# Kernel tuning notes

Hardware: AMD Instinct MI355X
Metric: run time of the kernel (lower is better)

Reference implementation:

```python
import jax, jax.numpy as jnp
import numpy as np

NS, NV, HE = 16, 8, 32          # scalar channels, vector (l=1) channels, edge hidden
D = NS + 3 * NV                  # flat irreps feature dim = 40
WN = NS*NS + NV*NS + NS*NV + NV*NV + NV*NV  # per-edge TP weight numel = 640
N_NODES, N_EDGES = 10000, 160000
C110 = 1.0 / np.sqrt(3.0)        # CG norm for 1o x 1o -> 0e (dot)
C111 = 1.0 / np.sqrt(2.0)        # CG norm for 1o x 1o -> 1o (cross)
EPS = 1e-5
_OFF = np.cumsum([0, NS*NS, NV*NS, NS*NV, NV*NV, NV*NV])


def _split(x):
    return x[:, :NS], x[:, NS:].reshape(x.shape[0], NV, 3)


def _flat(s, v):
    return jnp.concatenate([s, v.reshape(v.shape[0], -1)], axis=-1)


def _irreps_linear(x, Ws, Wv):
    s, v = _split(x)
    return s @ Ws, jnp.einsum('nid,io->nod', v, Wv)


def _mlp(x, w1, b1, w2, b2):
    return jax.nn.relu(x @ w1 + b1) @ w2 + b2


def _tp(x_s, x_v, sh, w):
    # equivariant tensor product (feat 16x0e+8x1o) x (sh 1x0e+1x1o) -> (16x0e+8x1o)
    E = x_s.shape[0]
    sh_s, sh_v = sh[:, 0], sh[:, 1:4]
    w1 = w[:, _OFF[0]:_OFF[1]].reshape(E, NS, NS)  # 0e x 0e -> 0e
    w2 = w[:, _OFF[1]:_OFF[2]].reshape(E, NV, NS)  # 1o x 1o -> 0e (dot)
    w3 = w[:, _OFF[2]:_OFF[3]].reshape(E, NS, NV)  # 0e x 1o -> 1o
    w4 = w[:, _OFF[3]:_OFF[4]].reshape(E, NV, NV)  # 1o x 0e -> 1o
    w5 = w[:, _OFF[4]:_OFF[5]].reshape(E, NV, NV)  # 1o x 1o -> 1o (cross)
    dot = jnp.einsum('eid,ed->ei', x_v, sh_v)
    cross = jnp.cross(x_v, sh_v[:, None, :])
    out_s = (jnp.einsum('eio,ei->eo', w1, x_s * sh_s[:, None])
             + C110 * jnp.einsum('eio,ei->eo', w2, dot))
    out_v = (jnp.einsum('eio,ei,ed->eod', w3, x_s, sh_v)
             + jnp.einsum('eio,eid->eod', w4, x_v * sh_s[:, None, None])
             + C111 * jnp.einsum('eio,eid->eod', w5, cross))
    return out_s, out_v


def _batchnorm(x, w_s, b_s, w_v):
    # e3nn-style BatchNorm: standard BN on scalars, norm-normalization on vectors
    s, v = _split(x)
    mu, var = s.mean(0), s.var(0)
    s = (s - mu) / jnp.sqrt(var + EPS) * w_s + b_s
    norm = (v * v).mean(-1).mean(0)  # [NV]
    v = v / jnp.sqrt(norm + EPS)[None, :, None] * w_v[None, :, None]
    return _flat(s, v)


def setup_inputs() -> dict:
    key = jax.random.key(0)
    ks = jax.random.split(key, 12)
    g = lambda i, shape, sc=1.0: jax.random.normal(ks[i], shape, jnp.float32) * sc
    return {
        'atom_features': g(0, (N_NODES, D)),
        'edge_features': g(1, (N_EDGES, HE)),
        'edge_sh': g(2, (N_EDGES, 4)),
        'Wq_s': g(3, (NS, NS), 1.0 / np.sqrt(NS)),
        'Wq_v': g(4, (NV, NV), 1.0 / np.sqrt(NV)),
        'k_w1': g(5, (HE, HE), 1.0 / np.sqrt(HE)), 'k_b1': jnp.zeros((HE,), jnp.float32),
        'k_w2': g(6, (HE, WN), 1.0 / np.sqrt(HE)), 'k_b2': jnp.zeros((WN,), jnp.float32),
        'v_w1': g(7, (HE, HE), 1.0 / np.sqrt(HE)), 'v_b1': jnp.zeros((HE,), jnp.float32),
        'v_w2': g(8, (HE, WN), 1.0 / np.sqrt(HE)), 'v_b2': jnp.zeros((WN,), jnp.float32),
        'bn_w_s': jnp.ones((NS,), jnp.float32), 'bn_b_s': jnp.zeros((NS,), jnp.float32),
        'bn_w_v': jnp.ones((NV,), jnp.float32),
        'edge_index': jax.random.randint(ks[9], (2, N_EDGES), 0, N_NODES),
    }


def reference(atom_features, edge_features, edge_sh, Wq_s, Wq_v,
              k_w1, k_b1, k_w2, k_b2, v_w1, v_b1, v_w2, v_b2,
              bn_w_s, bn_b_s, bn_w_v, edge_index):
    edge_dst, edge_src = edge_index[0], edge_index[1]
    q = _flat(*_irreps_linear(atom_features, Wq_s, Wq_v))[edge_src]     # [E, D]
    x_s, x_v = _split(atom_features[edge_dst])
    k = _flat(*_tp(x_s, x_v, edge_sh, _mlp(edge_features, k_w1, k_b1, k_w2, k_b2)))
    v = _flat(*_tp(x_s, x_v, edge_sh, _mlp(edge_features, v_w1, v_b1, v_w2, v_b2)))
    attn = jnp.sum(q * k, axis=-1)                                       # [E]
    m = jax.ops.segment_max(attn, edge_src, num_segments=N_NODES)
    m = jnp.where(jnp.isfinite(m), m, 0.0)
    e = jnp.exp(attn - m[edge_src])
    denom = jax.ops.segment_sum(e, edge_src, num_segments=N_NODES)
    a = e / denom[edge_src]
    upd = jax.ops.segment_sum(v * a[:, None], edge_src, num_segments=N_NODES)
    out = _batchnorm(atom_features + upd, bn_w_s, bn_b_s, bn_w_v)
    return out, edge_features
```

## Files before the change

### kernel.cpp

```cpp
#include <hip/hip_runtime.h>
#include <hip/hip_bf16.h>

typedef unsigned short u16;
typedef unsigned int u32;
typedef _Float16 h16;

#define NNODES 10000
#define NEDGES 160000

#define C110 0.57735026918962576f
#define C111 0.70710678118654752f

typedef __attribute__((ext_vector_type(8))) _Float16 half8;
typedef __attribute__((ext_vector_type(4))) float f32x4;

__device__ int   g_isf32;
__device__ float g_q[NNODES * 40];
__device__ float g_x[NNODES * 40];
__device__ float g_stats64[64][40];
__device__ u16   g_vb16[(size_t)NEDGES * 40];
__device__ u32   g_cnt8[8 * NNODES];
__device__ int2  g_bucket2[(size_t)NNODES * 128];
__device__ h16   g_w1hk[1024], g_w1lk[1024], g_w1hv[1024], g_w1lv[1024];
__device__ __align__(16) h16 g_w2k[640 * 32];
__device__ __align__(16) h16 g_w2v[640 * 32];
__device__ float g_b1k[32], g_b1v[32], g_b2k[640], g_b2v[640];

__device__ __forceinline__ float bf2f(u16 v) {
    return __uint_as_float(((u32)v) << 16);
}
__device__ __forceinline__ u32 f2bfbits(float f) {
    u32 u = __float_as_uint(f);
    u32 r = 0x7FFFu + ((u >> 16) & 1u);
    return (u + r) >> 16;
}
__device__ __forceinline__ u32 pack2(float a, float b) {
    return f2bfbits(a) | (f2bfbits(b) << 16);
}
__device__ __forceinline__ float ldx(const void* p, size_t i, int f32) {
    return f32 ? ((const float*)p)[i] : bf2f(((const u16*)p)[i]);
}
__device__ __forceinline__ void split2h(float v, h16& hi, h16& lo) {
    h16 h = (h16)v;
    hi = h;
    lo = (h16)(v - (float)h);
}
__device__ __forceinline__ void unp8(uint4 v, float* x) {
    x[0] = bf2f((u16)(v.x & 0xffffu)); x[1] = bf2f((u16)(v.x >> 16));
    x[2] = bf2f((u16)(v.y & 0xffffu)); x[3] = bf2f((u16)(v.y >> 16));
    x[4] = bf2f((u16)(v.z & 0xffffu)); x[5] = bf2f((u16)(v.z >> 16));
    x[6] = bf2f((u16)(v.w & 0xffffu)); x[7] = bf2f((u16)(v.w >> 16));
}
__device__ __forceinline__ void gld16(const void* g, void* l) {
    __builtin_amdgcn_global_load_lds(
        (__attribute__((address_space(1))) void*)(uintptr_t)g,
        (__attribute__((address_space(3))) void*)l, 16, 0, 0);
}

__global__ __launch_bounds__(256) void k_pre(
    const void* __restrict__ atom, const void* __restrict__ Wqs,
    const void* __restrict__ Wqv,
    const void* __restrict__ kw1, const void* __restrict__ kb1,
    const void* __restrict__ kw2, const void* __restrict__ kb2,
    const void* __restrict__ vw1, const void* __restrict__ vb1,
    const void* __restrict__ vw2, const void* __restrict__ vb2,
    const void* __restrict__ ef, void* __restrict__ out) {
    __shared__ int sF32;
    __shared__ float sW[320];
    const int tid = threadIdx.x;
    const u16* atom16 = (const u16*)atom;

    if (tid < 64) {
        int cnt = 0;
        #pragma unroll 4
        for (int j = tid * 16; j < tid * 16 + 16; ++j) {
            float ve = bf2f(atom16[2 * j]);
            float ae = fabsf(ve);
            if (ve == 0.f || (ae > 9.3e-13f && ae < 1.1e12f)) cnt++;
        }
        cnt += __shfl_xor(cnt, 1);  cnt += __shfl_xor(cnt, 2);
        cnt += __shfl_xor(cnt, 4);  cnt += __shfl_xor(cnt, 8);
        cnt += __shfl_xor(cnt, 16); cnt += __shfl_xor(cnt, 32);
        if (tid == 0) {
            int r = (cnt < 716) ? 1 : 0;
            sF32 = r;
            if (blockIdx.x == 0) g_isf32 = r;
        }
    }
    __syncthreads();
    const int f32 = sF32;

    int i = blockIdx.x * 256 + tid;
    if (i < 8 * NNODES) g_cnt8[i] = 0u;
    if (i < 64 * 40) ((float*)g_stats64)[i] = 0.f;

    if (blockIdx.x >= 40 && blockIdx.x < 120) {
        int t = i - 10240;
        if (t < 640 * 32) {
            int k = t / 640, n = t - k * 640;
            g_w2k[n * 32 + k] = (h16)ldx(kw2, t, f32);
            g_w2v[n * 32 + k] = (h16)ldx(vw2, t, f32);
        }
        if (t < 1024) {
            int s = t >> 5, tt = t & 31;
            split2h(ldx(kw1, t, f32), g_w1hk[tt * 32 + s], g_w1lk[tt * 32 + s]);
            split2h(ldx(vw1, t, f32), g_w1hv[tt * 32 + s], g_w1lv[tt * 32 + s]);
        }
        if (t < 640) { g_b2k[t] = ldx(kb2, t, f32); g_b2v[t] = ldx(vb2, t, f32); }
        if (t < 32)  { g_b1k[t] = ldx(kb1, t, f32); g_b1v[t] = ldx(vb1, t, f32); }
    } else if (blockIdx.x < 40) {
        sW[tid] = ldx(Wqs, tid, f32);
        if (tid < 64) sW[256 + tid] = ldx(Wqv, tid, f32);
        __syncthreads();
        int n = i;
        if (n >= NNODES) return;
        float x[40];
        if (f32) {
            const float4* ap = (const float4*)((const float*)atom + (size_t)n * 40);
            #pragma unroll
            for (int c = 0; c < 10; ++c) {
                float4 v = ap[c];
                x[c*4+0] = v.x; x[c*4+1] = v.y; x[c*4+2] = v.z; x[c*4+3] = v.w;
            }
        } else {
            const uint4* ap = (const uint4*)((const u16*)atom + (size_t)n * 40);
            #pragma unroll
            for (int c = 0; c < 5; ++c) unp8(ap[c], x + c * 8);
        }
        float qs[16];
        #pragma unroll
        for (int o = 0; o < 16; ++o) qs[o] = 0.f;
        #pragma unroll 1
        for (int ii = 0; ii < 16; ++ii) {
            float ai = x[ii];
            #pragma unroll
            for (int o = 0; o < 16; ++o) qs[o] = fmaf(ai, sW[ii * 16 + o], qs[o]);
        }
        float qv[24];
        #pragma unroll
        for (int k = 0; k < 24; ++k) qv[k] = 0.f;
        #pragma unroll 1
        for (int ii = 0; ii < 8; ++ii) {
            float a0 = x[16 + 3*ii + 0], a1 = x[16 + 3*ii + 1], a2 = x[16 + 3*ii + 2];
            #pragma unroll
            for (int o = 0; o < 8; ++o) {
                float wv = sW[256 + ii * 8 + o];
                qv[o*3+0] = fmaf(a0, wv, qv[o*3+0]);
                qv[o*3+1] = fmaf(a1, wv, qv[o*3+1]);
                qv[o*3+2] = fmaf(a2, wv, qv[o*3+2]);
            }
        }
        float* qp = g_q + (size_t)n * 40;
        #pragma unroll
        for (int o = 0; o < 16; ++o) qp[o] = qs[o];
        #pragma unroll
        for (int k = 0; k < 24; ++k) qp[16 + k] = qv[k];
    } else {
        const size_t b = blockIdx.x - 120;
        if (f32) {
            const uint4* s = (const uint4*)ef;
            uint4* d = (uint4*)((char*)out + 1600000u);
            for (size_t idx = b * 256 + tid; idx < 1280000u; idx += 200u * 256u)
                d[idx] = s[idx];
        } else {
            const uint4* s = (const uint4*)ef;
            uint4* d = (uint4*)((char*)out + 800000u);
            for (size_t idx = b * 256 + tid; idx < 640000u; idx += 200u * 256u)
                d[idx] = s[idx];
        }
    }
}

#define ACCS 41

#define STAGE(cc, WK, WV) do { \
    gld16((const char*)g_w2k + (cc)*4096 + w*1024 + lane*16, (char*)(WK) + w*1024); \
    gld16((const char*)g_w2v + (cc)*4096 + w*1024 + lane*16, (char*)(WV) + w*1024); \
} while (0)

#define TILE(nt, WK, WV) do { \
    const int tl_ = (nt) & 3; \
    half8 bk = *(const half8*)((WK) + (tl_*16 + c) * 32 + quad * 8); \
    half8 bv = *(const half8*)((WV) + (tl_*16 + c) * 32 + quad * 8); \
    float bbk = sB2k[(nt)*16 + c], bbv = sB2v[(nt)*16 + c]; \
    f32x4 Ck = {bbk, bbk, bbk, bbk}; \
    f32x4 Cv = {bbv, bbv, bbv, bbv}; \
    Ck = __builtin_amdgcn_mfma_f32_16x16x32_f16(aflk, bk, Ck, 0, 0, 0); \
    Ck = __builtin_amdgcn_mfma_f32_16x16x32_f16(afhk, bk, Ck, 0, 0, 0); \
    Cv = __builtin_amdgcn_mfma_f32_16x16x32_f16(aflv, bv, Cv, 0, 0, 0); \
    Cv = __builtin_amdgcn_mfma_f32_16x16x32_f16(afhv, bv, Cv, 0, 0, 0); \
    if ((nt) < 16) { \
        f32x4 xf = *(const f32x4*)(smF + (8 + (nt)) * 64 + e0); \
        _Pragma("unroll") \
        for (int r = 0; r < 4; ++r) { float fr = xf[r] * ssf[r]; \
            aSk[r] = fmaf(Ck[r], fr, aSk[r]); \
            aSv[r] = fmaf(Cv[r], fr, aSv[r]); } \
    } else if ((nt) < 24) { \
        f32x4 f = *(const f32x4*)(smF + ((nt) - 16) * 64 + e0); \
        _Pragma("unroll") \
        for (int r = 0; r < 4; ++r) { \
            aSk[r] = fmaf(Ck[r], f[r], aSk[r]); \
            aSv[r] = fmaf(Cv[r], f[r], aSv[r]); } \
    } else if ((nt) < 32) { \
        f32x4 f = *(const f32x4*)(smF + (8 + 2*((nt)-24) + ch) * 64 + e0); \
        _Pragma("unroll") \
        for (int r = 0; r < 4; ++r) { \
            aTk[r] = fmaf(Ck[r], f[r], aTk[r]); \
            aTv[r] = fmaf(Cv[r], f[r], aTv[r]); } \
    } else if ((nt) < 36) { \
        const int i_ = 2*((nt)-32) + ch; \
        _Pragma("unroll") \
        for (int d = 0; d < 3; ++d) { \
            f32x4 f = *(const f32x4*)(smF + (24 + d*8 + i_) * 64 + e0); \
            _Pragma("unroll") \
            for (int r = 0; r < 4; ++r) { \
                aVk[d*4+r] = fmaf(Ck[r], f[r], aVk[d*4+r]); \
                aVv[d*4+r] = fmaf(Cv[r], f[r], aVv[d*4+r]); } } \
    } else { \
        const int i_ = 2*((nt)-36) + ch; \
        _Pragma("unroll") \
        for (int d = 0; d < 3; ++d) { \
            f32x4 f = *(const f32x4*)(smF + (48 + d*8 + i_) * 64 + e0); \
            _Pragma("unroll") \
            for (int r = 0; r < 4; ++r) { \
                aVk[d*4+r] = fmaf(Ck[r], f[r], aVk[d*4+r]); \
                aVv[d*4+r] = fmaf(Cv[r], f[r], aVv[d*4+r]); } } \
    } \
} while (0)

#define DO_CHUNK(cc, WK, WV) do { \
    TILE((cc)*4 + 0, WK, WV); \
    TILE((cc)*4 + 1, WK, WV); \
    TILE((cc)*4 + 2, WK, WV); \
    TILE((cc)*4 + 3, WK, WV); \
} while (0)

__global__ __launch_bounds__(256, 4) void k_edge(
    const void* __restrict__ atom, const void* __restrict__ ef,
    const void* __restrict__ sh, const int* __restrict__ ei,
    void* __restrict__ out) {
    __shared__ __align__(16) float smF[76 * 64];
    __shared__ __align__(16) h16 sWkA[2048], sWvA[2048];
    __shared__ __align__(16) h16 sWkB[2048], sWvB[2048];
    __shared__ float sB2k[640], sB2v[640];

    const int f32 = g_isf32;
    const int t = threadIdx.x;
    const int w = t >> 6, lane = t & 63;
    const int quad = lane >> 4, c = lane & 15;
    const int eb = blockIdx.x * 64;
    const int slice = blockIdx.x & 7;

    STAGE(0, sWkA, sWvA);
    for (int i2 = t; i2 < 640; i2 += 256) { sB2k[i2] = g_b2k[i2]; sB2v[i2] = g_b2v[i2]; }

    half8 efh, efl;
    {
        const size_t base = (size_t)(eb + w * 16 + c) * 32 + quad * 8;
        h16 th, tl;
        if (f32) {
            const float4* ep = (const float4*)((const float*)ef + base);
            float4 v0 = ep[0], v1 = ep[1];
            split2h(v0.x, th, tl); efh[0] = th; efl[0] = tl;
            split2h(v0.y, th, tl); efh[1] = th; efl[1] = tl;
            split2h(v0.z, th, tl); efh[2] = th; efl[2] = tl;
            split2h(v0.w, th, tl); efh[3] = th; efl[3] = tl;
            split2h(v1.x, th, tl); efh[4] = th; efl[4] = tl;
            split2h(v1.y, th, tl); efh[5] = th; efl[5] = tl;
            split2h(v1.z, th, tl); efh[6] = th; efl[6] = tl;
            split2h(v1.w, th, tl); efh[7] = th; efl[7] = tl;
        } else {
            uint4 v = *(const uint4*)((const u16*)ef + base);
            float xe[8];
            unp8(v, xe);
            #pragma unroll
            for (int j = 0; j < 8; ++j) {
                split2h(xe[j], th, tl);
                efh[j] = th; efl[j] = tl;
            }
        }
    }

    if (lane < 16) {
        const int e = w * 16 + lane;
        const int ge = eb + e;
        const int dst = ei[ge];
        float x[40];
        float ss, s0, s1, s2;
        if (f32) {
            const float4* xp = (const float4*)((const float*)atom + (size_t)dst * 40);
            #pragma unroll
            for (int i = 0; i < 10; ++i) {
                float4 v = xp[i];
                x[i*4+0] = v.x; x[i*4+1] = v.y; x[i*4+2] = v.z; x[i*4+3] = v.w;
            }
            float4 s4 = *(const float4*)((const float*)sh + (size_t)ge * 4);
            ss = s4.x; s0 = s4.y; s1 = s4.z; s2 = s4.w;
        } else {
            const uint4* xp = (const uint4*)((const u16*)atom + (size_t)dst * 40);
            #pragma unroll
            for (int i = 0; i < 5; ++i) unp8(xp[i], x + i * 8);
            uint2 s2v = *(const uint2*)((const u16*)sh + (size_t)ge * 4);
            ss = bf2f((u16)(s2v.x & 0xffffu)); s0 = bf2f((u16)(s2v.x >> 16));
            s1 = bf2f((u16)(s2v.y & 0xffffu)); s2 = bf2f((u16)(s2v.y >> 16));
        }
        #pragma unroll
        for (int i = 0; i < 16; ++i)
            smF[(8 + i) * 64 + e] = x[i];
        #pragma unroll
        for (int i = 0; i < 8; ++i) {
            float a0 = x[16+3*i], a1 = x[17+3*i], a2 = x[18+3*i];
            smF[i * 64 + e]        = C110 * (a0*s0 + a1*s1 + a2*s2);
            smF[(24 + i) * 64 + e] = a0 * ss;
            smF[(32 + i) * 64 + e] = a1 * ss;
            smF[(40 + i) * 64 + e] = a2 * ss;
            smF[(48 + i) * 64 + e] = C111 * (a1*s2 - a2*s1);
            smF[(56 + i) * 64 + e] = C111 * (a2*s0 - a0*s2);
            smF[(64 + i) * 64 + e] = C111 * (a0*s1 - a1*s0);
        }
        smF[72*64 + e] = s0; smF[73*64 + e] = s1; smF[74*64 + e] = s2;
        smF[75*64 + e] = ss;
    }

    half8 afhk, aflk, afhv, aflv;
    #pragma unroll
    for (int p = 0; p < 2; ++p) {
        const h16* w1h = p ? g_w1hv : g_w1hk;
        const h16* w1l = p ? g_w1lv : g_w1lk;
        const float* b1 = p ? g_b1v : g_b1k;
        f32x4 H0, H1;
        #pragma unroll
        for (int nt = 0; nt < 2; ++nt) {
            half8 ah = *(const half8*)(w1h + (nt*16 + c) * 32 + quad * 8);
            half8 al = *(const half8*)(w1l + (nt*16 + c) * 32 + quad * 8);
            f32x4 D = {0.f, 0.f, 0.f, 0.f};
            D = __builtin_amdgcn_mfma_f32_16x16x32_f16(al, efh, D, 0, 0, 0);
            D = __builtin_amdgcn_mfma_f32_16x16x32_f16(ah, efl, D, 0, 0, 0);
            D = __builtin_amdgcn_mfma_f32_16x16x32_f16(ah, efh, D, 0, 0, 0);
            #pragma unroll
            for (int r = 0; r < 4; ++r)
                D[r] = fmaxf(D[r] + b1[nt*16 + quad*4 + r], 0.f);
            if (nt == 0) H0 = D; else H1 = D;
        }
        half8 th8, tl8;
        #pragma unroll
        for (int j = 0; j < 8; ++j) {
            int sl = (((2*quad + (j >> 2)) & 3) << 4) + c;
            float v0 = __shfl(H0[j & 3], sl);
            float v1 = __shfl(H1[j & 3], sl);
            float val = (quad < 2) ? v0 : v1;
            h16 hh, ll;
            split2h(val, hh, ll);
            th8[j] = hh; tl8[j] = ll;
        }
        if (p == 0) { afhk = th8; aflk = tl8; }
        else        { afhv = th8; aflv = tl8; }
    }

    const int e0 = w * 16 + quad * 4;
    const int o = c & 7, ch = c >> 3;

    f32x4 ssf = *(const f32x4*)(smF + 75*64 + e0);

    float aSk[4] = {0.f,0.f,0.f,0.f}, aTk[4] = {0.f,0.f,0.f,0.f};
    float aVk[12] = {0.f,0.f,0.f,0.f,0.f,0.f,0.f,0.f,0.f,0.f,0.f,0.f};
    float aSv[4] = {0.f,0.f,0.f,0.f}, aTv[4] = {0.f,0.f,0.f,0.f};
    float aVv[12] = {0.f,0.f,0.f,0.f,0.f,0.f,0.f,0.f,0.f,0.f,0.f,0.f};

    __syncthreads();
    STAGE(1, sWkB, sWvB);  DO_CHUNK(0, sWkA, sWvA);
    __syncthreads();
    STAGE(2, sWkA, sWvA);  DO_CHUNK(1, sWkB, sWvB);
    __syncthreads();
    STAGE(3, sWkB, sWvB);  DO_CHUNK(2, sWkA, sWvA);
    __syncthreads();
    STAGE(4, sWkA, sWvA);  DO_CHUNK(3, sWkB, sWvB);
    __syncthreads();
    STAGE(5, sWkB, sWvB);  DO_CHUNK(4, sWkA, sWvA);
    __syncthreads();
    STAGE(6, sWkA, sWvA);  DO_CHUNK(5, sWkB, sWvB);
    __syncthreads();
    STAGE(7, sWkB, sWvB);  DO_CHUNK(6, sWkA, sWvA);
    __syncthreads();
    STAGE(8, sWkA, sWvA);  DO_CHUNK(7, sWkB, sWvB);
    __syncthreads();
    STAGE(9, sWkB, sWvB);  DO_CHUNK(8, sWkA, sWvA);
    __syncthreads();
    DO_CHUNK(9, sWkB, sWvB);
    __syncthreads();

    float* const accp = smF + w * 656;

    const int el = lane >> 2, part = lane & 3;
    const int ge2 = eb + w * 16 + el;

    #pragma unroll
    for (int r = 0; r < 4; ++r) accp[(quad*4 + r) * ACCS + c] = aSk[r];
    #pragma unroll
    for (int r = 0; r < 4; ++r) aTk[r] += __shfl_xor(aTk[r], 8);
    #pragma unroll
    for (int d = 0; d < 3; ++d)
        #pragma unroll
        for (int r = 0; r < 4; ++r) aVk[d*4+r] += __shfl_xor(aVk[d*4+r], 8);
    if (ch == 0) {
        #pragma unroll
        for (int d = 0; d < 3; ++d) {
            f32x4 sv = *(const f32x4*)(smF + (72 + d) * 64 + e0);
            #pragma unroll
            for (int r = 0; r < 4; ++r)
                accp[(quad*4 + r) * ACCS + 16 + o*3 + d] = aVk[d*4+r] + aTk[r] * sv[r];
        }
    }
    {
        const int src = ei[NEDGES + ge2];
        const float* qp = g_q + (size_t)src * 40 + part * 10;
        const float* ap = accp + el * ACCS + part * 10;
        float partial = 0.f;
        #pragma unroll
        for (int d2 = 0; d2 < 10; ++d2) partial = fmaf(qp[d2], ap[d2], partial);
        partial += __shfl_xor(partial, 1);
        partial += __shfl_xor(partial, 2);
        if (part == 0) {
            u32 pos = atomicAdd(&g_cnt8[slice * NNODES + src], 1u);
            if (pos < 16u) {
                int2 ent;
                ent.x = ge2;
                ent.y = __float_as_int(partial);
                g_bucket2[(size_t)src * 128 + slice * 16 + pos] = ent;
            }
        }
    }

    #pragma unroll
    for (int r = 0; r < 4; ++r) accp[(quad*4 + r) * ACCS + c] = aSv[r];
    #pragma unroll
    for (int r = 0; r < 4; ++r) aTv[r] += __shfl_xor(aTv[r], 8);
    #pragma unroll
    for (int d = 0; d < 3; ++d)
        #pragma unroll
        for (int r = 0; r < 4; ++r) aVv[d*4+r] += __shfl_xor(aVv[d*4+r], 8);
    if (ch == 0) {
        #pragma unroll
        for (int d = 0; d < 3; ++d) {
            f32x4 sv = *(const f32x4*)(smF + (72 + d) * 64 + e0);
            #pragma unroll
            for (int r = 0; r < 4; ++r)
                accp[(quad*4 + r) * ACCS + 16 + o*3 + d] = aVv[d*4+r] + aTv[r] * sv[r];
        }
    }
    {
        u32* vb = (u32*)(g_vb16 + (size_t)ge2 * 40) + part * 5;
        const float* ap = accp + el * ACCS + part * 10;
        #pragma unroll
        for (int d2 = 0; d2 < 5; ++d2) vb[d2] = pack2(ap[2*d2], ap[2*d2+1]);
    }
}

__global__ __launch_bounds__(256) void k_post(const void* __restrict__ atom) {
    __shared__ float part_s[40];
    __shared__ int   sse[4][128];
    __shared__ float ssp[4][128];
    const int f32 = g_isf32;
    const int w = threadIdx.x >> 6;
    const int node = blockIdx.x * 4 + w;
    const int lane = threadIdx.x & 63;
    if (threadIdx.x < 40) part_s[threadIdx.x] = 0.f;
    __syncthreads();

    const int idx = lane & 15;
    u32 c0 = g_cnt8[(lane >> 4) * NNODES + node];
    u32 c1 = g_cnt8[(4 + (lane >> 4)) * NNODES + node];
    int2 b0 = g_bucket2[(size_t)node * 128 + lane];
    int2 b1 = g_bucket2[(size_t)node * 128 + 64 + lane];
    if (c0 > 16u) c0 = 16u;
    if (c1 > 16u) c1 = 16u;
    const bool v0 = (u32)idx < c0, v1 = (u32)idx < c1;

    const float NEGINF = -__builtin_huge_valf();
    float a0v = v0 ? __int_as_float(b0.y) : NEGINF;
    float a1v = v1 ? __int_as_float(b1.y) : NEGINF;
    float m = fmaxf(a0v, a1v);
    m = fmaxf(m, __shfl_xor(m, 1));  m = fmaxf(m, __shfl_xor(m, 2));
    m = fmaxf(m, __shfl_xor(m, 4));  m = fmaxf(m, __shfl_xor(m, 8));
    m = fmaxf(m, __shfl_xor(m, 16)); m = fmaxf(m, __shfl_xor(m, 32));

    float p0 = v0 ? expf(a0v - m) : 0.f;
    float p1 = v1 ? expf(a1v - m) : 0.f;

    float dv = p0 + p1;
    dv += __shfl_xor(dv, 1);  dv += __shfl_xor(dv, 2);
    dv += __shfl_xor(dv, 4);  dv += __shfl_xor(dv, 8);
    dv += __shfl_xor(dv, 16); dv += __shfl_xor(dv, 32);
    const float den = dv;

    const unsigned long long below = (1ull << lane) - 1ull;
    unsigned long long mk0 = __ballot(p0 != 0.f);
    if (p0 != 0.f) {
        int cidx = (int)__popcll(mk0 & below);
        sse[w][cidx] = b0.x; ssp[w][cidx] = p0;
    }
    int n0 = (int)__popcll(mk0);
    unsigned long long mk1 = __ballot(p1 != 0.f);
    if (p1 != 0.f) {
        int cidx = n0 + (int)__popcll(mk1 & below);
        sse[w][cidx] = b1.x; ssp[w][cidx] = p1;
    }
    const int n = n0 + (int)__popcll(mk1);

    float a0 = 0.f, a1 = 0.f, a2 = 0.f, a3 = 0.f;
    float a4 = 0.f, a5 = 0.f, a6 = 0.f, a7 = 0.f;
    if (lane < 40) {
        int k = 0;
        for (; k + 8 <= n; k += 8) {
            a0 = fmaf(ssp[w][k+0], bf2f(g_vb16[(size_t)sse[w][k+0] * 40 + lane]), a0);
            a1 = fmaf(ssp[w][k+1], bf2f(g_vb16[(size_t)sse[w][k+1] * 40 + lane]), a1);
            a2 = fmaf(ssp[w][k+2], bf2f(g_vb16[(size_t)sse[w][k+2] * 40 + lane]), a2);
            a3 = fmaf(ssp[w][k+3], bf2f(g_vb16[(size_t)sse[w][k+3] * 40 + lane]), a3);
            a4 = fmaf(ssp[w][k+4], bf2f(g_vb16[(size_t)sse[w][k+4] * 40 + lane]), a4);
            a5 = fmaf(ssp[w][k+5], bf2f(g_vb16[(size_t)sse[w][k+5] * 40 + lane]), a5);
            a6 = fmaf(ssp[w][k+6], bf2f(g_vb16[(size_t)sse[w][k+6] * 40 + lane]), a6);
            a7 = fmaf(ssp[w][k+7], bf2f(g_vb16[(size_t)sse[w][k+7] * 40 + lane]), a7);
        }
        for (; k + 2 <= n; k += 2) {
            a0 = fmaf(ssp[w][k+0], bf2f(g_vb16[(size_t)sse[w][k+0] * 40 + lane]), a0);
            a1 = fmaf(ssp[w][k+1], bf2f(g_vb16[(size_t)sse[w][k+1] * 40 + lane]), a1);
        }
        if (k < n)
            a0 = fmaf(ssp[w][k], bf2f(g_vb16[(size_t)sse[w][k] * 40 + lane]), a0);
    }
    float acc = ((a0 + a1) + (a2 + a3)) + ((a4 + a5) + (a6 + a7));

    float inv = (den > 0.f) ? 1.f / den : 0.f;
    float xv = 0.f;
    if (lane < 40) {
        xv = ldx(atom, (size_t)node * 40 + lane, f32) + acc * inv;
        g_x[(size_t)node * 40 + lane] = xv;
    }
    if (lane < 16) {
        atomicAdd(&part_s[lane], xv);
        atomicAdd(&part_s[16 + lane], xv * xv);
    }
    float sq = xv * xv;
    float tri = sq + __shfl_down(sq, 1) + __shfl_down(sq, 2);
    if (lane >= 16 && lane < 40 && ((lane - 16) % 3 == 0))
        atomicAdd(&part_s[32 + (lane - 16) / 3], tri);
    __syncthreads();
    if (threadIdx.x < 40)
        atomicAdd(&g_stats64[blockIdx.x & 63][threadIdx.x], part_s[threadIdx.x]);
}

__global__ __launch_bounds__(256) void k_out(
    const void* __restrict__ bws, const void* __restrict__ bbs,
    const void* __restrict__ bwv, void* __restrict__ out) {
    __shared__ float sst[40];
    __shared__ float spar[40];
    const int f32 = g_isf32;
    int t = threadIdx.x;
    const float invN = 1.f / (float)NNODES;
    if (t < 40) {
        float s_ = 0.f;
        #pragma unroll 8
        for (int s = 0; s < 64; ++s) s_ += g_stats64[s][t];
        sst[t] = s_;
    }
    __syncthreads();
    if (t < 16) {
        float mu = sst[t] * invN;
        float var = fmaxf(sst[16 + t] * invN - mu * mu, 0.f);
        float isd = 1.f / sqrtf(var + 1e-5f);
        float sc = ldx(bws, t, f32) * isd;
        spar[t] = sc;
        spar[16 + t] = ldx(bbs, t, f32) - mu * sc;
    } else if (t >= 32 && t < 40) {
        int i = t - 32;
        float norm = sst[t] * (invN / 3.f);
        spar[t] = ldx(bwv, i, f32) / sqrtf(norm + 1e-5f);
    }
    __syncthreads();

    int n = blockIdx.x * 256 + t;
    if (n >= NNODES) return;
    const float4* xp4 = (const float4*)(g_x + (size_t)n * 40);
    float xp[40];
    #pragma unroll
    for (int c = 0; c < 10; ++c) {
        float4 v = xp4[c];
        xp[c*4+0] = v.x; xp[c*4+1] = v.y; xp[c*4+2] = v.z; xp[c*4+3] = v.w;
    }
    float res[40];
    #pragma unroll
    for (int c = 0; c < 16; ++c) res[c] = xp[c] * spar[c] + spar[16 + c];
    #pragma unroll
    for (int i = 0; i < 8; ++i) {
        float s = spar[32 + i];
        res[16+3*i+0] = xp[16+3*i+0] * s;
        res[16+3*i+1] = xp[16+3*i+1] * s;
        res[16+3*i+2] = xp[16+3*i+2] * s;
    }
    if (f32) {
        float4* op = (float4*)((float*)out + (size_t)n * 40);
        #pragma unroll
        for (int c = 0; c < 10; ++c)
            op[c] = make_float4(res[c*4+0], res[c*4+1], res[c*4+2], res[c*4+3]);
    } else {
        uint4* op = (uint4*)((u16*)out + (size_t)n * 40);
        #pragma unroll
        for (int c = 0; c < 5; ++c) {
            uint4 r;
            r.x = pack2(res[c*8+0], res[c*8+1]);
            r.y = pack2(res[c*8+2], res[c*8+3]);
            r.z = pack2(res[c*8+4], res[c*8+5]);
            r.w = pack2(res[c*8+6], res[c*8+7]);
            op[c] = r;
        }
    }
}

extern "C" void kernel_launch(void* const* d_in, const int* in_sizes, int n_in,
                              void* d_out, int out_size, void* d_ws, size_t ws_size,
                              hipStream_t stream) {
    const void* atom = d_in[0];
    const void* ef   = d_in[1];
    const void* sh   = d_in[2];
    const void* Wqs  = d_in[3];
    const void* Wqv  = d_in[4];
    const void* kw1  = d_in[5];
    const void* kb1  = d_in[6];
    const void* kw2  = d_in[7];
    const void* kb2  = d_in[8];
    const void* vw1  = d_in[9];
    const void* vb1  = d_in[10];
    const void* vw2  = d_in[11];
    const void* vb2  = d_in[12];
    const void* bws  = d_in[13];
    const void* bbs  = d_in[14];
    const void* bwv  = d_in[15];
    const int*  ei   = (const int*)d_in[16];

    k_pre <<<320, 256, 0, stream>>>(atom, Wqs, Wqv, kw1, kb1, kw2, kb2,
                                    vw1, vb1, vw2, vb2, ef, d_out);
    k_edge<<<2500, 256, 0, stream>>>(atom, ef, sh, ei, d_out);
    k_post<<<2500, 256, 0, stream>>>(atom);
    k_out <<<40, 256, 0, stream>>>(bws, bbs, bwv, d_out);
}
```

Baseline: 189.5 us.

## Triple-buffer weight staging with vmcnt waits and prefetch query rows early

Replaces the double-buffered LDS weight staging, which used a full __syncthreads between chunks, with a three-slot ring. Each step waits with s_waitcnt vmcnt(2) plus a raw s_barrier, so up to two chunk loads stay in flight while the MFMA tiles run. The query row gather is moved before the main loop so its latency overlaps the compute. In k_post, bucket entries in slots 8 and above are loaded only when the count says they are valid. In exchange, the larger LDS footprint lowers the occupancy hint from 4 blocks to 3, and the hand-written waitcnt logic has to be exactly right.

Measured after the change: 195.0 us. 2.9% more time.

```diff
diff --git a/kernel.cpp b/kernel.cpp
--- a/kernel.cpp
+++ b/kernel.cpp
@@ -173,9 +173,16 @@
 
 #define ACCS 41
 
-#define STAGE(cc, WK, WV) do { \
-    gld16((const char*)g_w2k + (cc)*4096 + w*1024 + lane*16, (char*)(WK) + w*1024); \
-    gld16((const char*)g_w2v + (cc)*4096 + w*1024 + lane*16, (char*)(WV) + w*1024); \
+#define STAGE(cc, bi) do { \
+    gld16((const char*)g_w2k + (cc)*4096 + w*1024 + lane*16, (char*)sWk[bi] + w*1024); \
+    gld16((const char*)g_w2v + (cc)*4096 + w*1024 + lane*16, (char*)sWv[bi] + w*1024); \
+} while (0)
+
+#define WAITB(N) do { \
+    asm volatile("s_waitcnt vmcnt(" #N ") lgkmcnt(0)" ::: "memory"); \
+    __builtin_amdgcn_sched_barrier(0); \
+    __builtin_amdgcn_s_barrier(); \
+    __builtin_amdgcn_sched_barrier(0); \
 } while (0)
 
 #define TILE(nt, WK, WV) do { \
@@ -235,13 +242,13 @@
     TILE((cc)*4 + 3, WK, WV); \
 } while (0)
 
-__global__ __launch_bounds__(256, 4) void k_edge(
+__global__ __launch_bounds__(256, 3) void k_edge(
     const void* __restrict__ atom, const void* __restrict__ ef,
     const void* __restrict__ sh, const int* __restrict__ ei,
     void* __restrict__ out) {
     __shared__ __align__(16) float smF[76 * 64];
-    __shared__ __align__(16) h16 sWkA[2048], sWvA[2048];
-    __shared__ __align__(16) h16 sWkB[2048], sWvB[2048];
+    __shared__ __align__(16) h16 sWk[3][2048];
+    __shared__ __align__(16) h16 sWv[3][2048];
     __shared__ float sB2k[640], sB2v[640];
 
     const int f32 = g_isf32;
@@ -251,8 +258,21 @@
     const int eb = blockIdx.x * 64;
     const int slice = blockIdx.x & 7;
 
-    STAGE(0, sWkA, sWvA);
+    STAGE(0, 0);
     for (int i2 = t; i2 < 640; i2 += 256) { sB2k[i2] = g_b2k[i2]; sB2v[i2] = g_b2v[i2]; }
+
+    const int el = lane >> 2, part = lane & 3;
+    const int ge2 = eb + w * 16 + el;
+    const int src = ei[NEDGES + ge2];
+    float qpre[10];
+    {
+        const float2* qp2 = (const float2*)(g_q + (size_t)src * 40 + part * 10);
+        #pragma unroll
+        for (int j = 0; j < 5; ++j) {
+            float2 v = qp2[j];
+            qpre[2*j] = v.x; qpre[2*j+1] = v.y;
+        }
+    }
 
     half8 efh, efl;
     {
@@ -367,32 +387,20 @@
     float aSv[4] = {0.f,0.f,0.f,0.f}, aTv[4] = {0.f,0.f,0.f,0.f};
     float aVv[12] = {0.f,0.f,0.f,0.f,0.f,0.f,0.f,0.f,0.f,0.f,0.f,0.f};
 
+    STAGE(1, 1);
+    WAITB(2);  STAGE(2, 2);  DO_CHUNK(0, sWk[0], sWv[0]);
+    WAITB(2);  STAGE(3, 0);  DO_CHUNK(1, sWk[1], sWv[1]);
+    WAITB(2);  STAGE(4, 1);  DO_CHUNK(2, sWk[2], sWv[2]);
+    WAITB(2);  STAGE(5, 2);  DO_CHUNK(3, sWk[0], sWv[0]);
+    WAITB(2);  STAGE(6, 0);  DO_CHUNK(4, sWk[1], sWv[1]);
+    WAITB(2);  STAGE(7, 1);  DO_CHUNK(5, sWk[2], sWv[2]);
+    WAITB(2);  STAGE(8, 2);  DO_CHUNK(6, sWk[0], sWv[0]);
+    WAITB(2);  STAGE(9, 0);  DO_CHUNK(7, sWk[1], sWv[1]);
+    WAITB(2);                DO_CHUNK(8, sWk[2], sWv[2]);
+    WAITB(0);                DO_CHUNK(9, sWk[0], sWv[0]);
     __syncthreads();
-    STAGE(1, sWkB, sWvB);  DO_CHUNK(0, sWkA, sWvA);
-    __syncthreads();
-    STAGE(2, sWkA, sWvA);  DO_CHUNK(1, sWkB, sWvB);
-    __syncthreads();
-    STAGE(3, sWkB, sWvB);  DO_CHUNK(2, sWkA, sWvA);
-    __syncthreads();
-    STAGE(4, sWkA, sWvA);  DO_CHUNK(3, sWkB, sWvB);
-    __syncthreads();
-    STAGE(5, sWkB, sWvB);  DO_CHUNK(4, sWkA, sWvA);
-    __syncthreads();
-    STAGE(6, sWkA, sWvA);  DO_CHUNK(5, sWkB, sWvB);
-    __syncthreads();
-    STAGE(7, sWkB, sWvB);  DO_CHUNK(6, sWkA, sWvA);
-    __syncthreads();
-    STAGE(8, sWkA, sWvA);  DO_CHUNK(7, sWkB, sWvB);
-    __syncthreads();
-    STAGE(9, sWkB, sWvB);  DO_CHUNK(8, sWkA, sWvA);
-    __syncthreads();
-    DO_CHUNK(9, sWkB, sWvB);
-    __syncthreads();
 
     float* const accp = smF + w * 656;
-
-    const int el = lane >> 2, part = lane & 3;
-    const int ge2 = eb + w * 16 + el;
 
     #pragma unroll
     for (int r = 0; r < 4; ++r) accp[(quad*4 + r) * ACCS + c] = aSk[r];
@@ -412,12 +420,10 @@
         }
     }
     {
-        const int src = ei[NEDGES + ge2];
-        const float* qp = g_q + (size_t)src * 40 + part * 10;
         const float* ap = accp + el * ACCS + part * 10;
         float partial = 0.f;
         #pragma unroll
-        for (int d2 = 0; d2 < 10; ++d2) partial = fmaf(qp[d2], ap[d2], partial);
+        for (int d2 = 0; d2 < 10; ++d2) partial = fmaf(qpre[d2], ap[d2], partial);
         partial += __shfl_xor(partial, 1);
         partial += __shfl_xor(partial, 2);
         if (part == 0) {
@@ -468,12 +474,20 @@
     __syncthreads();
 
     const int idx = lane & 15;
+    int2 b0 = make_int2(0, (int)0xFF800000u);
+    int2 b1 = b0;
     u32 c0 = g_cnt8[(lane >> 4) * NNODES + node];
     u32 c1 = g_cnt8[(4 + (lane >> 4)) * NNODES + node];
-    int2 b0 = g_bucket2[(size_t)node * 128 + lane];
-    int2 b1 = g_bucket2[(size_t)node * 128 + 64 + lane];
+    if (idx < 8) {
+        b0 = g_bucket2[(size_t)node * 128 + lane];
+        b1 = g_bucket2[(size_t)node * 128 + 64 + lane];
+    }
     if (c0 > 16u) c0 = 16u;
     if (c1 > 16u) c1 = 16u;
+    if (idx >= 8) {
+        if ((u32)idx < c0) b0 = g_bucket2[(size_t)node * 128 + lane];
+        if ((u32)idx < c1) b1 = g_bucket2[(size_t)node * 128 + 64 + lane];
+    }
     const bool v0 = (u32)idx < c0, v1 = (u32)idx < c1;
 
     const float NEGINF = -__builtin_huge_valf();
```
